# Performance work log

Measured on AMD Instinct MI355X. Metric: run time of the kernel, lower is better.

The kernel has to match this reference:

```python
import jax, jax.numpy as jnp
import numpy as np

NUM_BITS = 16
BIT_START = 96
VALUE_DIM = 96  # E.DIM in the original code: the value payload slice [0:96)


def setup_inputs() -> dict:
    key = jax.random.key(0)
    B, S, D = 8, 32768, 128
    x = jax.random.normal(key, (B, S, D), dtype=jnp.float32)
    return {"x": x, "query_addr": 12345}


def reference(x, query_addr):
    # query_addr is a static Python int -> decompose into NUM_BITS binary bits
    query_bits = jnp.array([(query_addr >> k) & 1 for k in range(NUM_BITS)],
                           dtype=x.dtype)  # [NUM_BITS]
    key_bits = x[:, :, BIT_START:BIT_START + NUM_BITS]          # [B, S, NUM_BITS]
    match = 1.0 - jnp.abs(key_bits - query_bits)                # broadcast over [B, S]
    attention_weights = jnp.prod(match, axis=-1)                # [B, S]
    values = x[:, :, :VALUE_DIM]                                # [B, S, VALUE_DIM]
    output = jnp.einsum('bs,bsd->bd', attention_weights, values)  # [B, VALUE_DIM]
    return output
```

## Files before the change

kernel.cpp:

```cpp
#include <hip/hip_runtime.h>


constexpr int B = 8;
constexpr int S = 32768;
constexpr int D4 = 32;
constexpr int VAL4 = 24;
constexpr int ROWS_PER_STEP = 8;
constexpr int BLOCKS_PER_B = 256;
constexpr int SPB = S / BLOCKS_PER_B;

__global__ __launch_bounds__(256)
void bma_kernel(const float* __restrict__ x, const int* __restrict__ qaddr,
                float* __restrict__ out) {
    const int t    = threadIdx.x;
    const int c    = t & 31;
    const int rg   = t >> 5;
    const int lane = t & 63;
    const int b    = blockIdx.x / BLOCKS_PER_B;
    const int s0   = (blockIdx.x % BLOCKS_PER_B) * SPB;

    const unsigned qa = (unsigned)qaddr[0];
    float qb0 = 0.f, qb1 = 0.f, qb2 = 0.f, qb3 = 0.f;
    if (c >= 24 && c < 28) {
        const int k0 = (c - 24) * 4;
        qb0 = (float)((qa >> (k0 + 0)) & 1u);
        qb1 = (float)((qa >> (k0 + 1)) & 1u);
        qb2 = (float)((qa >> (k0 + 2)) & 1u);
        qb3 = (float)((qa >> (k0 + 3)) & 1u);
    }

    const float4* __restrict__ xb =
        reinterpret_cast<const float4*>(x) + (long)b * S * D4;
    const int src = (lane & 32) | 24;

    float4 acc = make_float4(0.f, 0.f, 0.f, 0.f);

    for (int s = s0 + rg; s < s0 + SPB; s += ROWS_PER_STEP) {
        float4 v = make_float4(0.f, 0.f, 0.f, 0.f);
        if (c < 28) v = xb[(long)s * D4 + c];

        float p = 1.0f;
        if (c >= 24 && c < 28) {
            p = (1.0f - fabsf(v.x - qb0)) * (1.0f - fabsf(v.y - qb1)) *
                (1.0f - fabsf(v.z - qb2)) * (1.0f - fabsf(v.w - qb3));
        }
        p *= __shfl_xor(p, 1);
        p *= __shfl_xor(p, 2);
        const float w = __shfl(p, src, 64);

        if (c < VAL4) {
            acc.x = fmaf(w, v.x, acc.x);
            acc.y = fmaf(w, v.y, acc.y);
            acc.z = fmaf(w, v.z, acc.z);
            acc.w = fmaf(w, v.w, acc.w);
        }
    }

    __shared__ float4 red[256];
    red[t] = acc;
    __syncthreads();
    if (t < 32) {
        float4 sum = red[t];
        #pragma unroll
        for (int g = 1; g < 8; ++g) {
            float4 o = red[t + 32 * g];
            sum.x += o.x; sum.y += o.y; sum.z += o.z; sum.w += o.w;
        }
        if (t < VAL4) {
            float* op = out + b * 96 + t * 4;
            atomicAdd(op + 0, sum.x);
            atomicAdd(op + 1, sum.y);
            atomicAdd(op + 2, sum.z);
            atomicAdd(op + 3, sum.w);
        }
    }
}

extern "C" void kernel_launch(void* const* d_in, const int* in_sizes, int n_in,
                              void* d_out, int out_size, void* d_ws, size_t ws_size,
                              hipStream_t stream) {
    const float* x  = (const float*)d_in[0];
    const int*   qa = (const int*)d_in[1];
    float*       out = (float*)d_out;

    hipMemsetAsync(out, 0, (size_t)out_size * sizeof(float), stream);

    bma_kernel<<<dim3(B * BLOCKS_PER_B), dim3(256), 0, stream>>>(x, qa, out);
}
```

Measured before the change: 213.0 us.

## Replace atomic output accumulation with two-stage partial-sum reduction

Per-block partial sums now go to a workspace buffer instead of being atomically added into the output. A second small kernel then reduces the 256 partials per batch and writes the result directly, so the memset goes away. The main loop is also rewritten with a fixed trip count and unroll 4 so more loads can be in flight. This adds a second kernel launch and relies on the workspace being large enough.

```diff
diff --git a/kernel.cpp b/kernel.cpp
--- a/kernel.cpp
+++ b/kernel.cpp
@@ -10,8 +10,8 @@
 constexpr int SPB = S / BLOCKS_PER_B;
 
 __global__ __launch_bounds__(256)
-void bma_kernel(const float* __restrict__ x, const int* __restrict__ qaddr,
-                float* __restrict__ out) {
+void bma_stage1(const float* __restrict__ x, const int* __restrict__ qaddr,
+                float* __restrict__ partial) {
     const int t    = threadIdx.x;
     const int c    = t & 31;
     const int rg   = t >> 5;
@@ -35,7 +35,9 @@
 
     float4 acc = make_float4(0.f, 0.f, 0.f, 0.f);
 
-    for (int s = s0 + rg; s < s0 + SPB; s += ROWS_PER_STEP) {
+    #pragma unroll 4
+    for (int i = 0; i < SPB / ROWS_PER_STEP; ++i) {
+        const int s = s0 + rg + i * ROWS_PER_STEP;
         float4 v = make_float4(0.f, 0.f, 0.f, 0.f);
         if (c < 28) v = xb[(long)s * D4 + c];
 
@@ -67,23 +69,53 @@
             sum.x += o.x; sum.y += o.y; sum.z += o.z; sum.w += o.w;
         }
         if (t < VAL4) {
-            float* op = out + b * 96 + t * 4;
-            atomicAdd(op + 0, sum.x);
-            atomicAdd(op + 1, sum.y);
-            atomicAdd(op + 2, sum.z);
-            atomicAdd(op + 3, sum.w);
+            float4* pp = reinterpret_cast<float4*>(partial) + (long)blockIdx.x * VAL4 + t;
+            *pp = sum;
         }
+    }
+}
+
+__global__ __launch_bounds__(256)
+void bma_stage2(const float* __restrict__ partial, float* __restrict__ out) {
+    const int t  = threadIdx.x;
+    const int c  = t & 31;
+    const int rg = t >> 5;
+    const int b  = blockIdx.x;
+
+    const float4* __restrict__ pp =
+        reinterpret_cast<const float4*>(partial) + (long)b * BLOCKS_PER_B * VAL4;
+
+    float4 acc = make_float4(0.f, 0.f, 0.f, 0.f);
+    if (c < VAL4) {
+        #pragma unroll 4
+        for (int chunk = rg; chunk < BLOCKS_PER_B; chunk += ROWS_PER_STEP) {
+            float4 v = pp[(long)chunk * VAL4 + c];
+            acc.x += v.x; acc.y += v.y; acc.z += v.z; acc.w += v.w;
+        }
+    }
+
+    __shared__ float4 red[256];
+    red[t] = acc;
+    __syncthreads();
+    if (t < VAL4) {
+        float4 sum = red[t];
+        #pragma unroll
+        for (int g = 1; g < 8; ++g) {
+            float4 o = red[t + 32 * g];
+            sum.x += o.x; sum.y += o.y; sum.z += o.z; sum.w += o.w;
+        }
+        reinterpret_cast<float4*>(out)[(long)b * VAL4 + t] = sum;
     }
 }
 
 extern "C" void kernel_launch(void* const* d_in, const int* in_sizes, int n_in,
                               void* d_out, int out_size, void* d_ws, size_t ws_size,
                               hipStream_t stream) {
-    const float* x  = (const float*)d_in[0];
-    const int*   qa = (const int*)d_in[1];
+    const float* x   = (const float*)d_in[0];
+    const int*   qa  = (const int*)d_in[1];
     float*       out = (float*)d_out;
+    float*       ws  = (float*)d_ws;
 
-    hipMemsetAsync(out, 0, (size_t)out_size * sizeof(float), stream);
-
-    bma_kernel<<<dim3(B * BLOCKS_PER_B), dim3(256), 0, stream>>>(x, qa, out);
+    bma_stage1<<<dim3(B * BLOCKS_PER_B), dim3(256), 0, stream>>>(x, qa, ws);
+    bma_stage2<<<dim3(B), dim3(256), 0, stream>>>(ws, out);
 }
```

After: 193.5 us. 1.1x faster.
